# Performance work log

Measured on AMD Instinct MI355X. Metric: run time of the kernel, lower is better.

## Reference

```python
import jax, jax.numpy as jnp
import numpy as np
import math

B, C, D, H, W = 2, 512, 8, 16, 16
HEADS = 8
HEAD_DIM = C // HEADS
GROUPS = 8
NUM_BUCKETS = 32
MAX_DIST = 128.0
EPS = 1e-5


def setup_inputs() -> dict:
    key = jax.random.key(0)
    ks = jax.random.split(key, 4)
    return {
        "x": jax.random.normal(ks[0], (B, C, D, H, W), dtype=jnp.float32),
        "gn_w": jnp.ones((C,), jnp.float32),
        "gn_b": jnp.zeros((C,), jnp.float32),
        "qkv_w": jax.random.normal(ks[1], (3 * C, C), dtype=jnp.float32) * 0.02,
        "qkv_b": jnp.zeros((3 * C,), jnp.float32),
        "proj_w": jax.random.normal(ks[2], (C, C), dtype=jnp.float32) * 0.02,
        "proj_b": jnp.zeros((C,), jnp.float32),
        "rel_emb": jax.random.normal(ks[3], (NUM_BUCKETS,), dtype=jnp.float32) * 0.02,
    }


def _rel_pos_bias(rel_emb):
    # 3D coords flattened in (d, h, w) order, matching torch meshgrid indexing='ij'
    dd, hh, ww = jnp.meshgrid(jnp.arange(D), jnp.arange(H), jnp.arange(W), indexing='ij')
    coords = jnp.stack([dd.ravel(), hh.ravel(), ww.ravel()], axis=-1).astype(jnp.float32)  # [N,3]
    rel = coords[:, None, :] - coords[None, :, :]                      # [N,N,3]
    dist = jnp.sqrt(jnp.sum(rel * rel, axis=-1))                       # euclidean distance
    buckets = jnp.clip(jnp.floor(dist / (MAX_DIST / NUM_BUCKETS)).astype(jnp.int32), 0, NUM_BUCKETS - 1)
    return rel_emb[buckets]                                            # [N,N]


def reference(x, gn_w, gn_b, qkv_w, qkv_b, proj_w, proj_b, rel_emb):
    N = D * H * W
    # GroupNorm(8, C)
    xr = x.reshape(B, GROUPS, C // GROUPS, N)
    mu = jnp.mean(xr, axis=(2, 3), keepdims=True)
    var = jnp.var(xr, axis=(2, 3), keepdims=True)
    h = ((xr - mu) * jax.lax.rsqrt(var + EPS)).reshape(B, C, D, H, W)
    h = h * gn_w[None, :, None, None, None] + gn_b[None, :, None, None, None]
    # qkv 1x1 Conv3d == pointwise linear over channels
    qkv = jnp.einsum('bcdhw,oc->bodhw', h, qkv_w) + qkv_b[None, :, None, None, None]
    q, k, v = jnp.split(qkv, 3, axis=1)  # each [B,C,D,H,W]

    def to_heads(t):  # [B, (heads d), D,H,W] -> [B, heads, N, d]
        return t.reshape(B, HEADS, HEAD_DIM, N).transpose(0, 1, 3, 2)

    q, k, v = to_heads(q), to_heads(k), to_heads(v)
    attn = jnp.einsum('bhid,bhjd->bhij', q, k) / math.sqrt(HEAD_DIM)
    attn = attn + _rel_pos_bias(rel_emb)[None, None]
    attn = jax.nn.softmax(attn, axis=-1)
    out = jnp.einsum('bhij,bhjd->bhid', attn, v)
    out = out.transpose(0, 1, 3, 2).reshape(B, C, D, H, W)
    out = jnp.einsum('bcdhw,oc->bodhw', out, proj_w) + proj_b[None, :, None, None, None]
    return x + out
```

## Files before the change

kernel.cpp:

```cpp
#include <hip/hip_runtime.h>

typedef __attribute__((ext_vector_type(8))) __bf16 bfv8;
typedef __attribute__((ext_vector_type(4))) float f4v;
typedef __attribute__((ext_vector_type(4))) unsigned short us4v;
typedef __attribute__((ext_vector_type(8))) unsigned short us8v;

static __device__ __forceinline__ unsigned short f2bf(float f){
  union { float f; unsigned u; } v; v.f = f;
  unsigned r = v.u + 0x7fffu + ((v.u >> 16) & 1u);
  return (unsigned short)(r >> 16);
}

static __device__ __forceinline__ unsigned cvtpk(float a, float b){
  unsigned r;
  asm("v_cvt_pk_bf16_f32 %0, %1, %2" : "=v"(r) : "v"(a), "v"(b));
  return r;
}

static __device__ __forceinline__ f4v mfma16(bfv8 a, bfv8 b, f4v c){
  return __builtin_amdgcn_mfma_f32_16x16x32_bf16(a, b, c, 0, 0, 0);
}


__global__ __launch_bounds__(256) void k_cvtfrag2(const float* __restrict__ qkvw,
                                                  const float* __restrict__ projw,
                                                  unsigned short* __restrict__ WQF,
                                                  unsigned short* __restrict__ WPF){
  int bid = blockIdx.x;
  const float* src; unsigned short* dst; int i;
  if (bid < 768){ src = qkvw; dst = WQF; i = bid*256 + threadIdx.x; }
  else          { src = projw; dst = WPF; i = (bid-768)*256 + threadIdx.x; }
  int o = i >> 7, c4 = (i & 127) << 2;
  float4 v = *(const float4*)(src + (size_t)o*512 + c4);
  us4v w; w[0]=f2bf(v.x); w[1]=f2bf(v.y); w[2]=f2bf(v.z); w[3]=f2bf(v.w);
  size_t off = (size_t)(o>>4)*8192 + ((c4>>5)<<9) + (((c4>>3)&3)<<7) + ((o&15)<<3) + (c4&7);
  *(us4v*)(dst + off) = w;
}

__global__ __launch_bounds__(256) void k_gnstat(const float* __restrict__ x,
                                                float2* __restrict__ part){
  int bg = blockIdx.x >> 4, ch = blockIdx.x & 15;
  const float4* base = (const float4*)(x + (size_t)bg*131072 + (size_t)ch*8192);
  float s=0.f, ss=0.f;
  #pragma unroll
  for (int it=0; it<8; ++it){
    float4 v = base[threadIdx.x + it*256];
    s  += v.x+v.y+v.z+v.w;
    ss += v.x*v.x+v.y*v.y+v.z*v.z+v.w*v.w;
  }
  #pragma unroll
  for (int off=1; off<64; off<<=1){ s += __shfl_xor(s,off); ss += __shfl_xor(ss,off); }
  __shared__ float red[8];
  int wid = threadIdx.x >> 6, l = threadIdx.x & 63;
  if (l==0){ red[wid]=s; red[wid+4]=ss; }
  __syncthreads();
  if (threadIdx.x==0)
    part[blockIdx.x] = make_float2(red[0]+red[1]+red[2]+red[3],
                                   red[4]+red[5]+red[6]+red[7]);
}

__global__ __launch_bounds__(256) void k_gnnorm(const float* __restrict__ x,
                                                const float2* __restrict__ part,
                                                const float* __restrict__ gnw,
                                                const float* __restrict__ gnb,
                                                unsigned short* __restrict__ AF){
  int nt = blockIdx.x & 31, ct = (blockIdx.x>>5)&7, b = blockIdx.x>>8;
  __shared__ float2 sms;
  __shared__ unsigned short tile[64][68];
  int tid = threadIdx.x;
  if (tid == 0){
    int bg = b*8 + ct;
    float s=0.f, ss=0.f;
    for (int i=0;i<16;++i){ float2 p = part[bg*16+i]; s+=p.x; ss+=p.y; }
    float mean = s * (1.f/131072.f);
    float var  = ss * (1.f/131072.f) - mean*mean;
    sms = make_float2(mean, rsqrtf(var + 1e-5f));
  }
  __syncthreads();
  float mean = sms.x, rstd = sms.y;
  int c0 = ct*64, n0 = nt*64;
  #pragma unroll
  for (int pass=0; pass<4; ++pass){
    int i = (tid>>4) + pass*16;
    int fc = tid & 15;
    int c = c0 + i;
    float w  = gnw[c]*rstd;
    float bb = gnb[c] - mean*w;
    float4 v = *(const float4*)(x + ((size_t)(b*512+c))*2048 + n0 + fc*4);
    tile[i][fc*4+0] = f2bf(v.x*w+bb);
    tile[i][fc*4+1] = f2bf(v.y*w+bb);
    tile[i][fc*4+2] = f2bf(v.z*w+bb);
    tile[i][fc*4+3] = f2bf(v.w*w+bb);
  }
  __syncthreads();
  #pragma unroll
  for (int pass=0; pass<2; ++pass){
    int r  = (tid>>3) + pass*32;
    int c8 = tid & 7;
    us8v o;
    #pragma unroll
    for (int u=0;u<8;++u) o[u] = tile[c8*8+u][r];
    int n = n0 + r, c = c0 + c8*8;
    size_t off = (size_t)(b*128 + (n>>4))*8192 + ((c>>5)<<9) + (((c>>3)&3)<<7) + ((n&15)<<3);
    *(us8v*)(AF + off) = o;
  }
}

__global__ __launch_bounds__(256) void k_qkv(const unsigned short* __restrict__ AF,
                                             const unsigned short* __restrict__ WQF,
                                             const float* __restrict__ qb,
                                             unsigned short* __restrict__ Qh,
                                             unsigned short* __restrict__ KF,
                                             unsigned short* __restrict__ VF){
  int bid = blockIdx.x;
  int ot = bid % 12; int t2 = bid / 12; int nt = t2 & 31; int b = t2 >> 5;
  int tid = threadIdx.x, wid = tid>>6, l = tid&63, lr = l&15, lg = l>>4;
  int n0 = nt*64 + wid*16, o0 = ot*128;
  f4v acc[8];
  #pragma unroll
  for (int s=0;s<8;++s) acc[s] = (f4v){0.f,0.f,0.f,0.f};
  const unsigned short* arow = AF + (size_t)(b*128 + (n0>>4))*8192 + l*8;
  const unsigned short* brow = WQF + (size_t)(o0>>4)*8192 + l*8;
  #pragma unroll
  for (int kc=0;kc<16;++kc){
    bfv8 a = *(const bfv8*)(arow + kc*512);
    #pragma unroll
    for (int s=0;s<8;++s){
      bfv8 bb = *(const bfv8*)(brow + s*8192 + kc*512);
      acc[s] = mfma16(a, bb, acc[s]);
    }
  }
  #pragma unroll
  for (int s=0;s<8;++s){
    int o = o0 + s*16 + lr;
    float bias = qb[o];
    int seg = o >> 9, oo = o & 511, h = oo>>6, dd = oo&63;
    size_t hb = (size_t)(b*8+h)*131072;
    #pragma unroll
    for (int r=0;r<4;++r){
      int n = n0 + lg*4 + r;
      unsigned short val = f2bf(acc[s][r] + bias);
      if (seg==0)
        Qh[hb + (size_t)n*64 + dd] = val;
      else if (seg==1)
        KF[hb + (n>>4)*1024 + (dd>>5)*512 + ((dd>>3)&3)*128 + (n&15)*8 + (dd&7)] = val;
      else
        VF[hb + (n>>5)*2048 + (dd>>4)*512 + ((n>>3)&3)*128 + (dd&15)*8 + (n&7)] = val;
    }
  }
}

__global__ __launch_bounds__(256,4) void k_attn(const unsigned short* __restrict__ Qh,
                                                const unsigned short* __restrict__ KF,
                                                const unsigned short* __restrict__ VF,
                                                const float* __restrict__ rel,
                                                unsigned short* __restrict__ AOF){
  int did = blockIdx.x;
  int bh = (did & 7)*2 + ((did >> 9) & 1);
  int qt = (did >> 3) & 63;
  int tid = threadIdx.x, wid = tid>>6, l = tid&63, lr = l&15, lg = l>>4;
  __shared__ float slut[32];
  __shared__ __align__(16) char smem[33792];
  __shared__ float slsum[4][32];
  float (*sO)[32][66] = (float (*)[32][66])smem;
  if (tid < 32){
    int bkt = (tid>=1)+(tid>=4)+(tid>=9)+(tid>=16)+(tid>=25);
    slut[tid] = rel[bkt];
  }
  __syncthreads();
  int q0 = qt*32;
  int dq = q0 >> 8, hqA = (q0 >> 4) & 15, hqB = hqA + 1;
  int swsq[4];
  #pragma unroll
  for (int r=0;r<4;++r){ int sw = lr - (lg*4+r); swsq[r] = sw*sw; }
  const unsigned short* Qb = Qh + (size_t)bh*131072;
  const unsigned short* Kb = KF + (size_t)bh*131072;
  const unsigned short* Vb = VF + (size_t)bh*131072;
  bfv8 qf0A = *(const bfv8*)(Qb + (size_t)(q0+lr)*64 + lg*8);
  bfv8 qf1A = *(const bfv8*)(Qb + (size_t)(q0+lr)*64 + 32 + lg*8);
  bfv8 qf0B = *(const bfv8*)(Qb + (size_t)(q0+16+lr)*64 + lg*8);
  bfv8 qf1B = *(const bfv8*)(Qb + (size_t)(q0+16+lr)*64 + 32 + lg*8);
  f4v oA[4], oB[4];
  #pragma unroll
  for (int i2=0;i2<4;++i2){ oA[i2] = (f4v){0.f,0.f,0.f,0.f}; oB[i2] = (f4v){0.f,0.f,0.f,0.f}; }
  float lsA = 0.f, lsB = 0.f;
  char* pwA = smem + wid*4096;
  char* pwB = pwA + 2048;
  int swz = (lr&7)<<4;
  for (int it=0; it<8; ++it){
    int itg = wid*8 + it;
    f4v sa[4], sb[4];
    #pragma unroll
    for (int t=0;t<4;++t){ sa[t] = (f4v){0.f,0.f,0.f,0.f}; sb[t] = (f4v){0.f,0.f,0.f,0.f}; }
    #pragma unroll
    for (int t=0;t<4;++t){
      const unsigned short* kb = Kb + (size_t)(itg*4 + t)*1024 + l*8;
      bfv8 k0 = *(const bfv8*)kb;
      bfv8 k1 = *(const bfv8*)(kb + 512);
      sa[t] = mfma16(k0, qf0A, sa[t]);
      sa[t] = mfma16(k1, qf1A, sa[t]);
      sb[t] = mfma16(k0, qf0B, sb[t]);
      sb[t] = mfma16(k1, qf1B, sb[t]);
    }
    int dj = itg>>2; int sd = dq-dj; int sds = sd*sd;
    int hj0 = (itg&3)*4;
    #pragma unroll
    for (int t=0;t<4;++t){
      int sh = hqA - (hj0+t); int sdh = sds + sh*sh;
      float p0 = __expf(fmaf(sa[t][0], 0.125f, slut[(sdh+swsq[0])>>4]));
      float p1 = __expf(fmaf(sa[t][1], 0.125f, slut[(sdh+swsq[1])>>4]));
      float p2 = __expf(fmaf(sa[t][2], 0.125f, slut[(sdh+swsq[2])>>4]));
      float p3 = __expf(fmaf(sa[t][3], 0.125f, slut[(sdh+swsq[3])>>4]));
      lsA += (p0+p1)+(p2+p3);
      uint2 w; w.x = cvtpk(p0,p1); w.y = cvtpk(p2,p3);
      *(uint2*)(pwA + lr*128 + ((32*t + 8*lg) ^ swz)) = w;
    }
    #pragma unroll
    for (int t=0;t<4;++t){
      int sh = hqB - (hj0+t); int sdh = sds + sh*sh;
      float p0 = __expf(fmaf(sb[t][0], 0.125f, slut[(sdh+swsq[0])>>4]));
      float p1 = __expf(fmaf(sb[t][1], 0.125f, slut[(sdh+swsq[1])>>4]));
      float p2 = __expf(fmaf(sb[t][2], 0.125f, slut[(sdh+swsq[2])>>4]));
      float p3 = __expf(fmaf(sb[t][3], 0.125f, slut[(sdh+swsq[3])>>4]));
      lsB += (p0+p1)+(p2+p3);
      uint2 w; w.x = cvtpk(p0,p1); w.y = cvtpk(p2,p3);
      *(uint2*)(pwB + lr*128 + ((32*t + 8*lg) ^ swz)) = w;
    }
    #pragma unroll
    for (int kt=0;kt<2;++kt){
      bfv8 pfA = *(const bfv8*)(pwA + lr*128 + ((64*kt + 16*lg) ^ swz));
      bfv8 pfB = *(const bfv8*)(pwB + lr*128 + ((64*kt + 16*lg) ^ swz));
      const unsigned short* vb = Vb + (size_t)(itg*2 + kt)*2048 + l*8;
      #pragma unroll
      for (int d2=0;d2<4;++d2){
        bfv8 vf = *(const bfv8*)(vb + d2*512);
        oA[d2] = mfma16(pfA, vf, oA[d2]);
        oB[d2] = mfma16(pfB, vf, oB[d2]);
      }
    }
  }
  lsA += __shfl_xor(lsA, 16); lsA += __shfl_xor(lsA, 32);
  lsB += __shfl_xor(lsB, 16); lsB += __shfl_xor(lsB, 32);
  __syncthreads();
  #pragma unroll
  for (int r=0;r<4;++r){
    #pragma unroll
    for (int d2=0;d2<4;++d2){
      sO[wid][lg*4+r][d2*16+lr] = oA[d2][r];
      sO[wid][16+lg*4+r][d2*16+lr] = oB[d2][r];
    }
  }
  if (l < 16){ slsum[wid][lr] = lsA; slsum[wid][16+lr] = lsB; }
  __syncthreads();
  int b = bh>>3, h = bh&7;
  int col = tid & 63, r0 = tid >> 6;
  #pragma unroll
  for (int k=0;k<8;++k){
    int row = r0*8 + k;
    float os = sO[0][row][col] + sO[1][row][col] + sO[2][row][col] + sO[3][row][col];
    float ls = slsum[0][row] + slsum[1][row] + slsum[2][row] + slsum[3][row];
    int n = q0 + row;
    size_t off = (size_t)(b*128 + (n>>4))*8192 + (size_t)(h*2 + (col>>5))*512
               + ((col>>3)&3)*128 + ((n&15))*8 + (col&7);
    AOF[off] = f2bf(os/ls);
  }
}

__global__ __launch_bounds__(256) void k_proj(const unsigned short* __restrict__ AOF,
                                              const unsigned short* __restrict__ WPF,
                                              const float* __restrict__ pb,
                                              const float* __restrict__ x,
                                              float* __restrict__ out){
  int nt = blockIdx.x & 31, ot = (blockIdx.x>>5)&7, b = blockIdx.x>>8;
  int tid = threadIdx.x, wid = tid>>6, l = tid&63, lr = l&15, lg = l>>4;
  int o0 = ot*64 + wid*16, n0 = nt*64;
  f4v acc[4];
  #pragma unroll
  for (int t=0;t<4;++t) acc[t] = (f4v){0.f,0.f,0.f,0.f};
  const unsigned short* arow = WPF + (size_t)(o0>>4)*8192 + l*8;
  const unsigned short* brow = AOF + (size_t)(b*128 + (n0>>4))*8192 + l*8;
  #pragma unroll
  for (int kc=0;kc<16;++kc){
    bfv8 a = *(const bfv8*)(arow + kc*512);
    #pragma unroll
    for (int t=0;t<4;++t){
      bfv8 bb = *(const bfv8*)(brow + t*8192 + kc*512);
      acc[t] = mfma16(a, bb, acc[t]);
    }
  }
  #pragma unroll
  for (int r=0;r<4;++r){
    int o = o0 + lg*4 + r;
    float bias = pb[o];
    #pragma unroll
    for (int t=0;t<4;++t){
      int n = n0 + t*16 + lr;
      size_t idx = ((size_t)(b*512)+o)*2048 + n;
      out[idx] = acc[t][r] + bias + x[idx];
    }
  }
}

extern "C" void kernel_launch(void* const* d_in, const int* in_sizes, int n_in,
                              void* d_out, int out_size, void* d_ws, size_t ws_size,
                              hipStream_t stream){
  const float* x     = (const float*)d_in[0];
  const float* gnw   = (const float*)d_in[1];
  const float* gnb   = (const float*)d_in[2];
  const float* qkvw  = (const float*)d_in[3];
  const float* qkvb  = (const float*)d_in[4];
  const float* projw = (const float*)d_in[5];
  const float* projb = (const float*)d_in[6];
  const float* rel   = (const float*)d_in[7];
  float* out = (float*)d_out;
  char* ws = (char*)d_ws;
  float2* part           = (float2*)ws;
  unsigned short* WQF    = (unsigned short*)(ws + 4096);
  unsigned short* WPF    = (unsigned short*)(ws + 1576960);
  unsigned short* AF     = (unsigned short*)(ws + 2101248);
  unsigned short* Qh     = (unsigned short*)(ws + 6295552);
  unsigned short* KF     = (unsigned short*)(ws + 10489856);
  unsigned short* VF     = (unsigned short*)(ws + 14684160);
  unsigned short* AOF    = (unsigned short*)(ws + 18878464);

  hipLaunchKernelGGL(k_cvtfrag2, dim3(1024), dim3(256), 0, stream, qkvw, projw, WQF, WPF);
  hipLaunchKernelGGL(k_gnstat,   dim3(256),  dim3(256), 0, stream, x, part);
  hipLaunchKernelGGL(k_gnnorm,   dim3(512),  dim3(256), 0, stream, x, part, gnw, gnb, AF);
  hipLaunchKernelGGL(k_qkv,      dim3(768),  dim3(256), 0, stream, AF, WQF, qkvb, Qh, KF, VF);
  hipLaunchKernelGGL(k_attn,     dim3(1024), dim3(256), 0, stream, Qh, KF, VF, rel, AOF);
  hipLaunchKernelGGL(k_proj,     dim3(512),  dim3(256), 0, stream, AOF, WPF, projb, x, out);
}
```

Before: 86.19 us.

## Split attention keys across eight waves and use exp2 with prescaled logits

The attention kernel now runs 512 threads (8 waves), each covering 4 key chunks instead of 8, which doubles the key-dimension split and fully unrolls the inner loop. The cross-wave reduction changes from a parallel 4-way shared-memory sum to a serialized 8-step accumulate, with a barrier per step, into one smaller buffer. Softmax uses exp2 with the log2e factor folded into the scale and the bias LUT. This aims to raise parallelism and occupancy and to cut exp cost, but adds eight barriers and a serialized reduction at the end.

```diff
diff --git a/kernel.cpp b/kernel.cpp
--- a/kernel.cpp
+++ b/kernel.cpp
@@ -15,6 +15,14 @@
   unsigned r;
   asm("v_cvt_pk_bf16_f32 %0, %1, %2" : "=v"(r) : "v"(a), "v"(b));
   return r;
+}
+
+static __device__ __forceinline__ float fexp2(float x){
+#if __has_builtin(__builtin_amdgcn_exp2f)
+  return __builtin_amdgcn_exp2f(x);
+#else
+  return __expf(x * 0.69314718056f);
+#endif
 }
 
 static __device__ __forceinline__ f4v mfma16(bfv8 a, bfv8 b, f4v c){
@@ -150,22 +158,20 @@
   }
 }
 
-__global__ __launch_bounds__(256,4) void k_attn(const unsigned short* __restrict__ Qh,
-                                                const unsigned short* __restrict__ KF,
-                                                const unsigned short* __restrict__ VF,
-                                                const float* __restrict__ rel,
-                                                unsigned short* __restrict__ AOF){
+__global__ __launch_bounds__(512, 8) void k_attn(const unsigned short* __restrict__ Qh,
+                                                 const unsigned short* __restrict__ KF,
+                                                 const unsigned short* __restrict__ VF,
+                                                 const float* __restrict__ rel,
+                                                 unsigned short* __restrict__ AOF){
   int did = blockIdx.x;
   int bh = (did & 7)*2 + ((did >> 9) & 1);
   int qt = (did >> 3) & 63;
   int tid = threadIdx.x, wid = tid>>6, l = tid&63, lr = l&15, lg = l>>4;
   __shared__ float slut[32];
-  __shared__ __align__(16) char smem[33792];
-  __shared__ float slsum[4][32];
-  float (*sO)[32][66] = (float (*)[32][66])smem;
+  __shared__ __align__(16) char smem[32768];
   if (tid < 32){
     int bkt = (tid>=1)+(tid>=4)+(tid>=9)+(tid>=16)+(tid>=25);
-    slut[tid] = rel[bkt];
+    slut[tid] = rel[bkt] * 1.44269504f;
   }
   __syncthreads();
   int q0 = qt*32;
@@ -187,8 +193,9 @@
   char* pwA = smem + wid*4096;
   char* pwB = pwA + 2048;
   int swz = (lr&7)<<4;
-  for (int it=0; it<8; ++it){
-    int itg = wid*8 + it;
+  #pragma unroll
+  for (int it=0; it<4; ++it){
+    int itg = wid*4 + it;
     f4v sa[4], sb[4];
     #pragma unroll
     for (int t=0;t<4;++t){ sa[t] = (f4v){0.f,0.f,0.f,0.f}; sb[t] = (f4v){0.f,0.f,0.f,0.f}; }
@@ -207,10 +214,10 @@
     #pragma unroll
     for (int t=0;t<4;++t){
       int sh = hqA - (hj0+t); int sdh = sds + sh*sh;
-      float p0 = __expf(fmaf(sa[t][0], 0.125f, slut[(sdh+swsq[0])>>4]));
-      float p1 = __expf(fmaf(sa[t][1], 0.125f, slut[(sdh+swsq[1])>>4]));
-      float p2 = __expf(fmaf(sa[t][2], 0.125f, slut[(sdh+swsq[2])>>4]));
-      float p3 = __expf(fmaf(sa[t][3], 0.125f, slut[(sdh+swsq[3])>>4]));
+      float p0 = fexp2(fmaf(sa[t][0], 0.180336878f, slut[(sdh+swsq[0])>>4]));
+      float p1 = fexp2(fmaf(sa[t][1], 0.180336878f, slut[(sdh+swsq[1])>>4]));
+      float p2 = fexp2(fmaf(sa[t][2], 0.180336878f, slut[(sdh+swsq[2])>>4]));
+      float p3 = fexp2(fmaf(sa[t][3], 0.180336878f, slut[(sdh+swsq[3])>>4]));
       lsA += (p0+p1)+(p2+p3);
       uint2 w; w.x = cvtpk(p0,p1); w.y = cvtpk(p2,p3);
       *(uint2*)(pwA + lr*128 + ((32*t + 8*lg) ^ swz)) = w;
@@ -218,10 +225,10 @@
     #pragma unroll
     for (int t=0;t<4;++t){
       int sh = hqB - (hj0+t); int sdh = sds + sh*sh;
-      float p0 = __expf(fmaf(sb[t][0], 0.125f, slut[(sdh+swsq[0])>>4]));
-      float p1 = __expf(fmaf(sb[t][1], 0.125f, slut[(sdh+swsq[1])>>4]));
-      float p2 = __expf(fmaf(sb[t][2], 0.125f, slut[(sdh+swsq[2])>>4]));
-      float p3 = __expf(fmaf(sb[t][3], 0.125f, slut[(sdh+swsq[3])>>4]));
+      float p0 = fexp2(fmaf(sb[t][0], 0.180336878f, slut[(sdh+swsq[0])>>4]));
+      float p1 = fexp2(fmaf(sb[t][1], 0.180336878f, slut[(sdh+swsq[1])>>4]));
+      float p2 = fexp2(fmaf(sb[t][2], 0.180336878f, slut[(sdh+swsq[2])>>4]));
+      float p3 = fexp2(fmaf(sb[t][3], 0.180336878f, slut[(sdh+swsq[3])>>4]));
       lsB += (p0+p1)+(p2+p3);
       uint2 w; w.x = cvtpk(p0,p1); w.y = cvtpk(p2,p3);
       *(uint2*)(pwB + lr*128 + ((32*t + 8*lg) ^ swz)) = w;
@@ -242,27 +249,45 @@
   lsA += __shfl_xor(lsA, 16); lsA += __shfl_xor(lsA, 32);
   lsB += __shfl_xor(lsB, 16); lsB += __shfl_xor(lsB, 32);
   __syncthreads();
-  #pragma unroll
-  for (int r=0;r<4;++r){
-    #pragma unroll
-    for (int d2=0;d2<4;++d2){
-      sO[wid][lg*4+r][d2*16+lr] = oA[d2][r];
-      sO[wid][16+lg*4+r][d2*16+lr] = oB[d2][r];
-    }
-  }
-  if (l < 16){ slsum[wid][lr] = lsA; slsum[wid][16+lr] = lsB; }
-  __syncthreads();
+  float* sOf = (float*)smem;
+  float* sls = (float*)(smem + 32*68*4);
+  #pragma unroll 1
+  for (int p=0; p<8; ++p){
+    if (wid == p){
+      if (p == 0){
+        #pragma unroll
+        for (int r=0;r<4;++r){
+          #pragma unroll
+          for (int d2=0;d2<4;++d2){
+            sOf[(lg*4+r)*68 + d2*16+lr] = oA[d2][r];
+            sOf[(16+lg*4+r)*68 + d2*16+lr] = oB[d2][r];
+          }
+        }
+        if (l < 16){ sls[l] = lsA; sls[16+l] = lsB; }
+      } else {
+        #pragma unroll
+        for (int r=0;r<4;++r){
+          #pragma unroll
+          for (int d2=0;d2<4;++d2){
+            sOf[(lg*4+r)*68 + d2*16+lr] += oA[d2][r];
+            sOf[(16+lg*4+r)*68 + d2*16+lr] += oB[d2][r];
+          }
+        }
+        if (l < 16){ sls[l] += lsA; sls[16+l] += lsB; }
+      }
+    }
+    __syncthreads();
+  }
   int b = bh>>3, h = bh&7;
-  int col = tid & 63, r0 = tid >> 6;
-  #pragma unroll
-  for (int k=0;k<8;++k){
-    int row = r0*8 + k;
-    float os = sO[0][row][col] + sO[1][row][col] + sO[2][row][col] + sO[3][row][col];
-    float ls = slsum[0][row] + slsum[1][row] + slsum[2][row] + slsum[3][row];
+  int col = tid & 63, rw = tid >> 6;
+  #pragma unroll
+  for (int k=0;k<4;++k){
+    int row = rw*4 + k;
+    float v = sOf[row*68 + col] / sls[row];
     int n = q0 + row;
     size_t off = (size_t)(b*128 + (n>>4))*8192 + (size_t)(h*2 + (col>>5))*512
-               + ((col>>3)&3)*128 + ((n&15))*8 + (col&7);
-    AOF[off] = f2bf(os/ls);
+               + ((col>>3)&3)*128 + (n&15)*8 + (col&7);
+    AOF[off] = f2bf(v);
   }
 }
 
@@ -327,6 +352,6 @@
   hipLaunchKernelGGL(k_gnstat,   dim3(256),  dim3(256), 0, stream, x, part);
   hipLaunchKernelGGL(k_gnnorm,   dim3(512),  dim3(256), 0, stream, x, part, gnw, gnb, AF);
   hipLaunchKernelGGL(k_qkv,      dim3(768),  dim3(256), 0, stream, AF, WQF, qkvb, Qh, KF, VF);
-  hipLaunchKernelGGL(k_attn,     dim3(1024), dim3(256), 0, stream, Qh, KF, VF, rel, AOF);
+  hipLaunchKernelGGL(k_attn,     dim3(1024), dim3(512), 0, stream, Qh, KF, VF, rel, AOF);
   hipLaunchKernelGGL(k_proj,     dim3(512),  dim3(256), 0, stream, AOF, WPF, projb, x, out);
 }
```

After: 173.9 us. +101.8%, slower.
